# Performance work log

Measured on AMD Instinct MI355X. Metric: run time of the kernel, lower is better.

## Reference

```python
import jax, jax.numpy as jnp
import numpy as np

N_ATOMS = 50000
N_MOTIFS = 50000
N_INC = 600000
N_GRAPHS = 512
H = 64            # h_dim / node_fea_dim
MOTIF_DIM = 94    # motif hyperedge feature dim
HOUT = 128        # hout_dim
Z_DIM = 2 * H + MOTIF_DIM  # concat dim inside CHGConv
BN_EPS = 1e-5


def seg_mean(x, idx, num):
    s = jax.ops.segment_sum(x, idx, num_segments=num)
    c = jax.ops.segment_sum(jnp.ones((x.shape[0], 1), x.dtype), idx, num_segments=num)
    return s / jnp.maximum(c, 1.0)


def setup_inputs() -> dict:
    key = jax.random.key(0)
    ks = jax.random.split(key, 12)
    inp = {}
    inp['atom_z'] = jax.random.randint(ks[0], (N_ATOMS,), 0, 101)
    inp['motif_attr'] = jax.random.normal(ks[1], (N_MOTIFS, MOTIF_DIM), dtype=jnp.float32)
    inp['hyperedge_index'] = jax.random.randint(ks[2], (2, N_INC), 0, N_ATOMS)
    inp['batch'] = jnp.sort(jax.random.randint(ks[3], (N_ATOMS,), 0, N_GRAPHS))
    s = 0.05
    inp['embed_table'] = jax.random.normal(ks[4], (101, H), dtype=jnp.float32) * s
    inp['w_f'] = jax.random.normal(ks[5], (Z_DIM, H), dtype=jnp.float32) * s
    inp['b_f'] = jnp.zeros((H,), jnp.float32)
    inp['w_c'] = jax.random.normal(ks[6], (Z_DIM, H), dtype=jnp.float32) * s
    inp['b_c'] = jnp.zeros((H,), jnp.float32)
    inp['bn_gamma'] = jnp.ones((H,), jnp.float32)
    inp['bn_beta'] = jnp.zeros((H,), jnp.float32)
    inp['w_l1'] = jax.random.normal(ks[7], (H, HOUT), dtype=jnp.float32) * s
    inp['b_l1'] = jnp.zeros((HOUT,), jnp.float32)
    inp['w_out'] = jax.random.normal(ks[8], (HOUT, 1), dtype=jnp.float32) * s
    inp['b_out'] = jnp.zeros((1,), jnp.float32)
    return inp


def reference(atom_z, motif_attr, hyperedge_index, batch, embed_table,
              w_f, b_f, w_c, b_c, bn_gamma, bn_beta, w_l1, b_l1, w_out, b_out):
    # atom embedding lookup
    x = embed_table[atom_z]                       # [N_ATOMS, H]
    src = hyperedge_index[0]                      # atom indices per incidence
    hid = hyperedge_index[1]                      # motif hyperedge indices per incidence

    # CHGConv: aggregate node feats to hyperedges, gated CGCNN-style message, scatter back
    hx = seg_mean(x[src], hid, N_MOTIFS)          # [N_MOTIFS, H]
    z = jnp.concatenate([x[src], hx[hid], motif_attr[hid]], axis=1)  # [N_INC, 2H+94]
    msg = jax.nn.sigmoid(z @ w_f + b_f) * jax.nn.softplus(z @ w_c + b_c)
    out = seg_mean(msg, src, N_ATOMS)             # [N_ATOMS, H]

    # batch norm (training-mode batch stats) + residual, then outer relu
    mu = out.mean(0)
    var = out.var(0)
    out = (out - mu) / jnp.sqrt(var + BN_EPS) * bn_gamma + bn_beta
    x = jax.nn.relu(out + x)

    g = seg_mean(x, batch, N_GRAPHS)              # [N_GRAPHS, H]
    h = jax.nn.softplus(g @ w_l1 + b_l1)          # [N_GRAPHS, HOUT]
    return h @ w_out + b_out                      # [N_GRAPHS, 1]
```

## Files before the change

### kernel.cpp

```cpp
#include <hip/hip_runtime.h>
#include <hip/hip_bf16.h>
#include <hip/hip_fp16.h>
#include <math.h>

#define N_ATOMS  50000
#define N_MOTIFS 50000
#define N_SEG    (N_MOTIFS + N_ATOMS)
#define N_INC    600000
#define N_GRAPHS 512
#define H        64
#define MOTIF_DIM 94
#define KP       47
#define HOUT     128
#define BN_EPS   1e-5f
#define NZ       101
#define BCAP     64
#define NBINM    196
#define NBIN     392
#define BINCAP   4096
#define CHUNK    2048
#define NBLK_S   ((N_INC + CHUNK - 1) / CHUNK)
#define TL       16
#define NBLK_T   (N_MOTIFS / TL)
#define NREP     32

typedef _Float16 h2_t __attribute__((ext_vector_type(2)));
typedef float f32x2 __attribute__((ext_vector_type(2)));
__device__ __forceinline__ float fdot2(__half2 a, __half2 b, float c) {
    return __builtin_amdgcn_fdot2(*(h2_t*)&a, *(h2_t*)&b, c, false);
}

__device__ __forceinline__ float softplus_fast(float x) {
    return fmaxf(x, 0.0f) + __logf(1.0f + __expf(-fabsf(x)));
}
__device__ __forceinline__ float gate_f(float f, float c) {
    float sig = __builtin_amdgcn_rcpf(1.0f + __expf(-f));
    return sig * softplus_fast(c);
}

__global__ __launch_bounds__(256) void bin_scatter(const int* __restrict__ he,
                                                   const int* __restrict__ atom_z,
                                                   unsigned* __restrict__ bin_cnt,
                                                   unsigned* __restrict__ gbin) {
    __shared__ unsigned ecnt[NBIN];
    __shared__ unsigned ebase[NBIN];
    int tid = threadIdx.x;
    int e0 = blockIdx.x * CHUNK;
    int e1 = (e0 + CHUNK < N_INC) ? e0 + CHUNK : N_INC;
    for (int i = tid; i < NBIN; i += 256) ecnt[i] = 0;
    __syncthreads();
    for (int e = e0 + tid; e < e1; e += 256) {
        int s = he[e];
        int h = he[N_INC + e];
        atomicAdd(&ecnt[h >> 8], 1u);
        atomicAdd(&ecnt[NBINM + (s >> 8)], 1u);
    }
    __syncthreads();
    for (int i = tid; i < NBIN; i += 256) {
        unsigned c = ecnt[i];
        ebase[i] = c ? atomicAdd(&bin_cnt[i], c) : 0u;
        ecnt[i] = 0u;
    }
    __syncthreads();
    for (int e = e0 + tid; e < e1; e += 256) {
        int s = he[e];
        int h = he[N_INC + e];
        int az = atom_z[s];
        int bm = h >> 8;
        unsigned sm = ebase[bm] + atomicAdd(&ecnt[bm], 1u);
        if (sm < BINCAP)
            gbin[(size_t)bm * BINCAP + sm] = ((unsigned)(h & 255) << 16) | (unsigned)az;
        int ba = NBINM + (s >> 8);
        unsigned sa = ebase[ba] + atomicAdd(&ecnt[ba], 1u);
        if (sa < BINCAP)
            gbin[(size_t)ba * BINCAP + sa] = ((unsigned)(s & 255) << 16) | (unsigned)h;
    }
}

__global__ __launch_bounds__(256) void bin_build(const unsigned* __restrict__ bin_cnt,
                                                 const unsigned* __restrict__ gbin,
                                                 unsigned* __restrict__ cnt,
                                                 unsigned char* __restrict__ csr_m,
                                                 unsigned short* __restrict__ csr_a) {
    __shared__ unsigned short bkt[256 * BCAP];
    __shared__ unsigned cnts[256];
    int b = blockIdx.x;
    int tid = threadIdx.x;
    bool isM = b < NBINM;
    int seg0 = (isM ? b : (b - NBINM)) << 8;
    int lim = 50000 - seg0; if (lim > 256) lim = 256; if (lim < 0) lim = 0;
    cnts[tid] = 0u;
    __syncthreads();
    unsigned n = bin_cnt[b];
    if (n > BINCAP) n = BINCAP;
    for (unsigned k = tid; k < n; k += 256) {
        unsigned e = gbin[(size_t)b * BINCAP + k];
        unsigned loc = e >> 16, val = e & 0xFFFFu;
        unsigned slot = atomicAdd(&cnts[loc], 1u);
        if (slot < BCAP) bkt[loc * BCAP + slot] = (unsigned short)val;
    }
    __syncthreads();
    if (tid < lim) cnt[(isM ? seg0 : N_MOTIFS + seg0) + tid] = cnts[tid];
    if (isM) {
        for (int i = tid; i < lim * 16; i += 256) {
            int loc = i >> 4, w = i & 15;
            const unsigned short* sp = &bkt[loc * BCAP + 4 * w];
            unsigned v = (sp[0] & 0xffu) | ((sp[1] & 0xffu) << 8) |
                         ((sp[2] & 0xffu) << 16) | ((sp[3] & 0xffu) << 24);
            ((unsigned*)csr_m)[(size_t)(seg0 + loc) * 16 + w] = v;
        }
    } else {
        for (int i = tid; i < lim * 32; i += 256) {
            int loc = i >> 5, w = i & 31;
            const unsigned short* sp = &bkt[loc * BCAP + 2 * w];
            unsigned v = (unsigned)sp[0] | ((unsigned)sp[1] << 16);
            ((unsigned*)csr_a)[(size_t)(seg0 + loc) * 32 + w] = v;
        }
    }
}

__global__ __launch_bounds__(256) void aux_kernel(const float* __restrict__ table,
                                                  const float* __restrict__ w_f,
                                                  const float* __restrict__ w_c,
                                                  const float* __restrict__ b_f,
                                                  const float* __restrict__ b_c,
                                                  float* __restrict__ atab_fc,
                                                  __half* __restrict__ ptab_h,
                                                  __half2* __restrict__ w2_fc,
                                                  float* __restrict__ b_fc) {
    int t = threadIdx.x;
    int z = blockIdx.x;
    if (z >= NZ) {
        if (t < 128) {
            int sel = t & 1, col = t >> 1;
            b_fc[t] = (sel ? b_c : b_f)[col];
            const float* ws = sel ? w_c : w_f;
            for (int kp = 0; kp < KP; kp++)
                w2_fc[(size_t)kp * 128 + t] = __floats2half2_rn(
                    ws[(size_t)(2 * H + 2 * kp) * H + col],
                    ws[(size_t)(2 * H + 2 * kp + 1) * H + col]);
        }
        return;
    }
    __shared__ float trow[H];
    if (t < H) trow[t] = table[(size_t)z * H + t];
    __syncthreads();
    if (t < 128) {
        int sel = (t >= 64) ? 1 : 0;
        int jj = t & 63;
        const float* ws = sel ? w_c : w_f;
        float aacc = 0.0f, pacc = 0.0f;
        for (int k = 0; k < H; k++) {
            float tv = trow[k];
            aacc += tv * ws[(size_t)k * H + jj];
            pacc += tv * ws[(size_t)(H + k) * H + jj];
        }
        atab_fc[(size_t)z * 128 + jj * 2 + sel] = aacc;
        ptab_h[(size_t)z * 128 + jj * 2 + sel] = __float2half_rn(pacc);
    }
}

__global__ __launch_bounds__(256) void motif_fused(const unsigned* __restrict__ cnt,
                                                   const unsigned char* __restrict__ csr_m,
                                                   const __half2* __restrict__ ptab_h,
                                                   const float* __restrict__ motif_attr,
                                                   const __half2* __restrict__ w2_fc,
                                                   const float* __restrict__ b_fc,
                                                   __half2* __restrict__ m_fc) {
    __shared__ __half2 w_s[KP * 128];
    __shared__ __half2 z2[TL][KP];
    __shared__ int     ez[TL * BCAP];
    __shared__ float   invd[TL];
    __shared__ int     degs[TL];
    int tid = threadIdx.x;
    int m0 = blockIdx.x * TL;

    for (int k4 = tid; k4 < KP * 32; k4 += 256)
        ((uint4*)w_s)[k4] = ((const uint4*)w2_fc)[k4];
    {
        const int* src = (const int*)(csr_m + (size_t)m0 * BCAP);
        int w = src[tid];
        int b0 = tid * 4;
        ez[b0]     =  w        & 0xff;
        ez[b0 + 1] = (w >> 8)  & 0xff;
        ez[b0 + 2] = (w >> 16) & 0xff;
        ez[b0 + 3] = (w >> 24) & 0xff;
    }
    if (tid < TL) {
        int d = (int)cnt[m0 + tid];
        d = (d < BCAP) ? d : BCAP;
        degs[tid] = d;
        invd[tid] = 1.0f / fmaxf((float)d, 1.0f);
    }
    {
        const f32x2* ap = (const f32x2*)motif_attr;
        for (int idx = tid; idx < TL * KP; idx += 256) {
            int m = idx / KP, kp = idx % KP;
            f32x2 v = __builtin_nontemporal_load(&ap[(size_t)(m0 + m) * KP + kp]);
            z2[m][kp] = __floats2half2_rn(v.x, v.y);
        }
    }
    __syncthreads();

    const uint2* ptab_u2 = (const uint2*)ptab_h;
    int rg = tid >> 5;
    int cg = tid & 31;
    int q  = cg * 4;
    float4 bias4 = *(const float4*)(b_fc + q);

    float acc[2][4];
#pragma unroll
    for (int i = 0; i < 2; i++) {
        int r = rg * 2 + i;
        int lo = r * BCAP, d = degs[r];
        float g0 = 0.f, g1 = 0.f, g2 = 0.f, g3 = 0.f;
        int k = 0;
        for (; k + 8 <= d; k += 8) {
            int zz[8];
#pragma unroll
            for (int u = 0; u < 8; u++) zz[u] = ez[lo + k + u];
#pragma unroll
            for (int u = 0; u < 8; u++) {
                uint2 pr = ptab_u2[zz[u] * 32 + cg];
                float2 fa = __half22float2(*(__half2*)&pr.x);
                float2 fb = __half22float2(*(__half2*)&pr.y);
                g0 += fa.x; g1 += fa.y; g2 += fb.x; g3 += fb.y;
            }
        }
        for (; k < d; k++) {
            uint2 pr = ptab_u2[ez[lo + k] * 32 + cg];
            float2 fa = __half22float2(*(__half2*)&pr.x);
            float2 fb = __half22float2(*(__half2*)&pr.y);
            g0 += fa.x; g1 += fa.y; g2 += fb.x; g3 += fb.y;
        }
        float iv = invd[r];
        acc[i][0] = bias4.x + g0 * iv;
        acc[i][1] = bias4.y + g1 * iv;
        acc[i][2] = bias4.z + g2 * iv;
        acc[i][3] = bias4.w + g3 * iv;
    }

    {
        int r0 = rg * 2, r1 = r0 + 1;
#pragma unroll 4
        for (int kp = 0; kp < KP; kp++) {
            uint4 wr = *(const uint4*)(w_s + (size_t)kp * 128 + q);
            __half2 w0 = *(__half2*)&wr.x, w1 = *(__half2*)&wr.y;
            __half2 w2h = *(__half2*)&wr.z, w3 = *(__half2*)&wr.w;
            __half2 za = z2[r0][kp], zb = z2[r1][kp];
            acc[0][0] = fdot2(za, w0,  acc[0][0]);
            acc[0][1] = fdot2(za, w1,  acc[0][1]);
            acc[0][2] = fdot2(za, w2h, acc[0][2]);
            acc[0][3] = fdot2(za, w3,  acc[0][3]);
            acc[1][0] = fdot2(zb, w0,  acc[1][0]);
            acc[1][1] = fdot2(zb, w1,  acc[1][1]);
            acc[1][2] = fdot2(zb, w2h, acc[1][2]);
            acc[1][3] = fdot2(zb, w3,  acc[1][3]);
        }
    }
#pragma unroll
    for (int i = 0; i < 2; i++) {
        int gm = m0 + rg * 2 + i;
        m_fc[(size_t)gm * 64 + cg * 2]     = __floats2half2_rn(acc[i][0], acc[i][1]);
        m_fc[(size_t)gm * 64 + cg * 2 + 1] = __floats2half2_rn(acc[i][2], acc[i][3]);
    }
}

__global__ __launch_bounds__(256) void msg_gather(const unsigned* __restrict__ cnt,
                                                  const unsigned short* __restrict__ csr_a,
                                                  const int* __restrict__ atom_z,
                                                  const float2* __restrict__ atab_fc,
                                                  const __half2* __restrict__ m_fc,
                                                  float* __restrict__ out_mean,
                                                  float* __restrict__ bn_part) {
    int i = blockIdx.x * 4 + (threadIdx.x >> 6);
    int j = threadIdx.x & 63;
    int zi = __builtin_amdgcn_readfirstlane(atom_z[i]);
    float2 a = atab_fc[(size_t)zi * H + j];
    unsigned b = (unsigned)i * BCAP;
    int d = (int)__builtin_amdgcn_readfirstlane(cnt[N_MOTIFS + i]);
    d = (d < BCAP) ? d : BCAP;
    int dm1 = (d > 0) ? d - 1 : 0;
    float acc = 0.0f;
    for (int k = 0; k < d; k += 8) {
        int hh[8];
#pragma unroll
        for (int u = 0; u < 8; u++) {
            int o = k + u;
            hh[u] = (int)csr_a[b + (unsigned)((o < d) ? o : dm1)];
        }
        __half2 hv[8];
#pragma unroll
        for (int u = 0; u < 8; u++) hv[u] = m_fc[((unsigned)hh[u] << 6) + (unsigned)j];
#pragma unroll
        for (int u = 0; u < 8; u++)
            if (k + u < d) {
                float2 v = __half22float2(hv[u]);
                acc += gate_f(a.x + v.x, a.y + v.y);
            }
    }
    float v = acc / fmaxf((float)d, 1.0f);
    out_mean[(size_t)i * H + j] = v;
    __shared__ float ssum[256];
    __shared__ float ssq[256];
    ssum[threadIdx.x] = v; ssq[threadIdx.x] = v * v;
    __syncthreads();
    if (threadIdx.x < 64) {
        float* rep = bn_part + (size_t)(blockIdx.x & (NREP - 1)) * 128;
        atomicAdd(&rep[j],      ssum[j] + ssum[64 + j] + ssum[128 + j] + ssum[192 + j]);
        atomicAdd(&rep[64 + j], ssq[j]  + ssq[64 + j]  + ssq[128 + j]  + ssq[192 + j]);
    }
}

__global__ __launch_bounds__(256) void pool_head(const float* __restrict__ out_mean,
                                                 const float* __restrict__ bn_part,
                                                 const float* __restrict__ gamma,
                                                 const float* __restrict__ beta,
                                                 const int* __restrict__ atom_z,
                                                 const float* __restrict__ table,
                                                 const int* __restrict__ batch,
                                                 const float* __restrict__ w_l1,
                                                 const float* __restrict__ b_l1,
                                                 const float* __restrict__ w_out,
                                                 const float* __restrict__ b_out,
                                                 float* __restrict__ out) {
    int g = blockIdx.x;
    int tid = threadIdx.x;
    __shared__ int bounds[2];
    __shared__ float red[256];
    __shared__ float gv[H];
    __shared__ float red2[HOUT];
    __shared__ float bnred[128];
    if (tid < 2) {
        int target = g + tid;
        int lo = 0, hi = N_ATOMS;
        while (lo < hi) {
            int mid = (lo + hi) >> 1;
            if (batch[mid] < target) lo = mid + 1; else hi = mid;
        }
        bounds[tid] = lo;
    }
    if (tid < 128) {
        float s = 0.0f;
        for (int r = 0; r < NREP; r++) s += bn_part[(size_t)r * 128 + tid];
        bnred[tid] = s;
    }
    __syncthreads();
    int s = bounds[0], e = bounds[1];
    int j = tid & 63, w = tid >> 6;
    const float invN = 1.0f / (float)N_ATOMS;
    float mu = bnred[j] * invN;
    float var = bnred[64 + j] * invN - mu * mu;
    float rstd = 1.0f / sqrtf(var + BN_EPS);
    float gm = gamma[j], bt = beta[j];
    float acc = 0.0f;
    for (int i = s + w; i < e; i += 4) {
        float d = out_mean[(size_t)i * H + j];
        float xv = table[(size_t)atom_z[i] * H + j];
        float o = (d - mu) * rstd * gm + bt;
        acc += fmaxf(o + xv, 0.0f);
    }
    red[tid] = acc;
    __syncthreads();
    if (tid < 64)
        gv[j] = (red[j] + red[64 + j] + red[128 + j] + red[192 + j])
                / fmaxf((float)(e - s), 1.0f);
    __syncthreads();
    if (tid < HOUT) {
        float a2 = b_l1[tid];
        for (int k = 0; k < H; k++) a2 += gv[k] * w_l1[(size_t)k * HOUT + tid];
        red2[tid] = softplus_fast(a2) * w_out[tid];
    }
    __syncthreads();
    for (int st = 64; st > 0; st >>= 1) {
        if (tid < st) red2[tid] += red2[tid + st];
        __syncthreads();
    }
    if (tid == 0) out[g] = red2[0] + b_out[0];
}

extern "C" void kernel_launch(void* const* d_in, const int* in_sizes, int n_in,
                              void* d_out, int out_size, void* d_ws, size_t ws_size,
                              hipStream_t stream) {
    const int*   atom_z     = (const int*)  d_in[0];
    const float* motif_attr = (const float*)d_in[1];
    const int*   he         = (const int*)  d_in[2];
    const int*   batch      = (const int*)  d_in[3];
    const float* table      = (const float*)d_in[4];
    const float* w_f        = (const float*)d_in[5];
    const float* b_f        = (const float*)d_in[6];
    const float* w_c        = (const float*)d_in[7];
    const float* b_c        = (const float*)d_in[8];
    const float* gamma      = (const float*)d_in[9];
    const float* beta       = (const float*)d_in[10];
    const float* w_l1       = (const float*)d_in[11];
    const float* b_l1       = (const float*)d_in[12];
    const float* w_out      = (const float*)d_in[13];
    const float* b_out      = (const float*)d_in[14];
    float* out = (float*)d_out;

    float*    bn_part = (float*)d_ws;
    unsigned* bin_cnt = (unsigned*)(bn_part + NREP * 128);
    char*     zero_end = (char*)(bin_cnt + 400);
    unsigned* cnt     = (unsigned*)zero_end;
    unsigned* gbin    = cnt + N_SEG;
    unsigned char*  csr_m = (unsigned char*)(gbin + (size_t)NBIN * BINCAP);
    unsigned short* csr_a = (unsigned short*)(csr_m + (size_t)N_MOTIFS * BCAP);
    float*    atab_fc  = (float*)(csr_a + (size_t)N_ATOMS * BCAP);
    __half*   ptab_h   = (__half*)(atab_fc + (size_t)NZ * 128);
    __half2*  w2_fc    = (__half2*)(ptab_h + (size_t)NZ * 128);
    float*    b_fc     = (float*)(w2_fc + (size_t)KP * 128);
    __half2*  m_fc     = (__half2*)(b_fc + 128);
    float*    out_mean = (float*)(m_fc + (size_t)N_MOTIFS * 64);

    size_t zero_bytes = (size_t)(zero_end - (char*)d_ws);
    hipMemsetAsync(d_ws, 0, zero_bytes, stream);

    aux_kernel<<<NZ + 1, 256, 0, stream>>>(table, w_f, w_c, b_f, b_c,
                                           atab_fc, ptab_h, w2_fc, b_fc);
    bin_scatter<<<NBLK_S, 256, 0, stream>>>(he, atom_z, bin_cnt, gbin);
    bin_build<<<NBIN, 256, 0, stream>>>(bin_cnt, gbin, cnt, csr_m, csr_a);
    motif_fused<<<NBLK_T, 256, 0, stream>>>(cnt, csr_m, (const __half2*)ptab_h,
                                            motif_attr, w2_fc, b_fc, m_fc);
    msg_gather<<<N_ATOMS / 4, 256, 0, stream>>>(cnt, csr_a, atom_z,
                                                (const float2*)atab_fc,
                                                m_fc, out_mean, bn_part);
    pool_head<<<N_GRAPHS, 256, 0, stream>>>(out_mean, bn_part, gamma, beta,
                                            atom_z, table, batch,
                                            w_l1, b_l1, w_out, b_out, out);
}
```

Baseline: 228.1 us.

## Fuse aux precompute into bin scatter and use base-2 gate math

The separate aux_kernel launch is folded into the bin_scatter kernel as extra blocks, removing one kernel launch and its serialization. The gate/weight tables are pre-scaled by log2(e) so the message gate can use native exp2/log2 intrinsics, with a final multiply by ln2 applied once per atom. The gather loop also predicates the index and message loads instead of clamping to the last valid index. The pre-scaling changes fp16 rounding slightly. Motif_fused must consume the scaled tables consistently, and that code is not shown.

```diff
diff --git a/kernel.cpp b/kernel.cpp
--- a/kernel.cpp
+++ b/kernel.cpp
@@ -23,6 +23,8 @@
 #define TL       16
 #define NBLK_T   (N_MOTIFS / TL)
 #define NREP     32
+#define LOG2E    1.44269504088896f
+#define LN2      0.69314718055995f
 
 typedef _Float16 h2_t __attribute__((ext_vector_type(2)));
 typedef float f32x2 __attribute__((ext_vector_type(2)));
@@ -33,18 +35,62 @@
 __device__ __forceinline__ float softplus_fast(float x) {
     return fmaxf(x, 0.0f) + __logf(1.0f + __expf(-fabsf(x)));
 }
-__device__ __forceinline__ float gate_f(float f, float c) {
-    float sig = __builtin_amdgcn_rcpf(1.0f + __expf(-f));
-    return sig * softplus_fast(c);
-}
-
-__global__ __launch_bounds__(256) void bin_scatter(const int* __restrict__ he,
-                                                   const int* __restrict__ atom_z,
-                                                   unsigned* __restrict__ bin_cnt,
-                                                   unsigned* __restrict__ gbin) {
+__device__ __forceinline__ float gate2(float f, float c) {
+    float e   = __builtin_amdgcn_exp2f(-f);
+    float sig = __builtin_amdgcn_rcpf(1.0f + e);
+    float ec  = __builtin_amdgcn_exp2f(-fabsf(c));
+    float sp  = fmaxf(c, 0.0f) + __builtin_amdgcn_logf(1.0f + ec);
+    return sig * sp;
+}
+
+__global__ __launch_bounds__(256) void bin_scatter_aux(const int* __restrict__ he,
+                                                       const int* __restrict__ atom_z,
+                                                       unsigned* __restrict__ bin_cnt,
+                                                       unsigned* __restrict__ gbin,
+                                                       const float* __restrict__ table,
+                                                       const float* __restrict__ w_f,
+                                                       const float* __restrict__ w_c,
+                                                       const float* __restrict__ b_f,
+                                                       const float* __restrict__ b_c,
+                                                       float* __restrict__ atab_fc,
+                                                       __half* __restrict__ ptab_h,
+                                                       __half2* __restrict__ w2_fc,
+                                                       float* __restrict__ b_fc) {
     __shared__ unsigned ecnt[NBIN];
     __shared__ unsigned ebase[NBIN];
+    __shared__ float trow[H];
     int tid = threadIdx.x;
+    if (blockIdx.x >= NBLK_S) {
+        int z = blockIdx.x - NBLK_S;
+        if (z >= NZ) {
+            if (tid < 128) {
+                int sel = tid & 1, col = tid >> 1;
+                b_fc[tid] = (sel ? b_c : b_f)[col] * LOG2E;
+                const float* ws = sel ? w_c : w_f;
+                for (int kp = 0; kp < KP; kp++)
+                    w2_fc[(size_t)kp * 128 + tid] = __floats2half2_rn(
+                        ws[(size_t)(2 * H + 2 * kp) * H + col] * LOG2E,
+                        ws[(size_t)(2 * H + 2 * kp + 1) * H + col] * LOG2E);
+            }
+            return;
+        }
+        if (tid < H) trow[tid] = table[(size_t)z * H + tid];
+        __syncthreads();
+        if (tid < 128) {
+            int sel = (tid >= 64) ? 1 : 0;
+            int jj = tid & 63;
+            const float* ws = sel ? w_c : w_f;
+            float aacc = 0.0f, pacc = 0.0f;
+            for (int k = 0; k < H; k++) {
+                float tv = trow[k];
+                aacc += tv * ws[(size_t)k * H + jj];
+                pacc += tv * ws[(size_t)(H + k) * H + jj];
+            }
+            atab_fc[(size_t)z * 128 + jj * 2 + sel] = aacc * LOG2E;
+            ptab_h[(size_t)z * 128 + jj * 2 + sel] = __float2half_rn(pacc * LOG2E);
+        }
+        return;
+    }
     int e0 = blockIdx.x * CHUNK;
     int e1 = (e0 + CHUNK < N_INC) ? e0 + CHUNK : N_INC;
     for (int i = tid; i < NBIN; i += 256) ecnt[i] = 0;
@@ -116,47 +162,6 @@
             unsigned v = (unsigned)sp[0] | ((unsigned)sp[1] << 16);
             ((unsigned*)csr_a)[(size_t)(seg0 + loc) * 32 + w] = v;
         }
-    }
-}
-
-__global__ __launch_bounds__(256) void aux_kernel(const float* __restrict__ table,
-                                                  const float* __restrict__ w_f,
-                                                  const float* __restrict__ w_c,
-                                                  const float* __restrict__ b_f,
-                                                  const float* __restrict__ b_c,
-                                                  float* __restrict__ atab_fc,
-                                                  __half* __restrict__ ptab_h,
-                                                  __half2* __restrict__ w2_fc,
-                                                  float* __restrict__ b_fc) {
-    int t = threadIdx.x;
-    int z = blockIdx.x;
-    if (z >= NZ) {
-        if (t < 128) {
-            int sel = t & 1, col = t >> 1;
-            b_fc[t] = (sel ? b_c : b_f)[col];
-            const float* ws = sel ? w_c : w_f;
-            for (int kp = 0; kp < KP; kp++)
-                w2_fc[(size_t)kp * 128 + t] = __floats2half2_rn(
-                    ws[(size_t)(2 * H + 2 * kp) * H + col],
-                    ws[(size_t)(2 * H + 2 * kp + 1) * H + col]);
-        }
-        return;
-    }
-    __shared__ float trow[H];
-    if (t < H) trow[t] = table[(size_t)z * H + t];
-    __syncthreads();
-    if (t < 128) {
-        int sel = (t >= 64) ? 1 : 0;
-        int jj = t & 63;
-        const float* ws = sel ? w_c : w_f;
-        float aacc = 0.0f, pacc = 0.0f;
-        for (int k = 0; k < H; k++) {
-            float tv = trow[k];
-            aacc += tv * ws[(size_t)k * H + jj];
-            pacc += tv * ws[(size_t)(H + k) * H + jj];
-        }
-        atab_fc[(size_t)z * 128 + jj * 2 + sel] = aacc;
-        ptab_h[(size_t)z * 128 + jj * 2 + sel] = __float2half_rn(pacc);
     }
 }
 
@@ -280,26 +285,24 @@
     unsigned b = (unsigned)i * BCAP;
     int d = (int)__builtin_amdgcn_readfirstlane(cnt[N_MOTIFS + i]);
     d = (d < BCAP) ? d : BCAP;
-    int dm1 = (d > 0) ? d - 1 : 0;
     float acc = 0.0f;
     for (int k = 0; k < d; k += 8) {
         int hh[8];
-#pragma unroll
-        for (int u = 0; u < 8; u++) {
-            int o = k + u;
-            hh[u] = (int)csr_a[b + (unsigned)((o < d) ? o : dm1)];
-        }
         __half2 hv[8];
 #pragma unroll
-        for (int u = 0; u < 8; u++) hv[u] = m_fc[((unsigned)hh[u] << 6) + (unsigned)j];
+        for (int u = 0; u < 8; u++)
+            if (k + u < d) hh[u] = (int)csr_a[b + (unsigned)(k + u)];
+#pragma unroll
+        for (int u = 0; u < 8; u++)
+            if (k + u < d) hv[u] = m_fc[((unsigned)hh[u] << 6) + (unsigned)j];
 #pragma unroll
         for (int u = 0; u < 8; u++)
             if (k + u < d) {
                 float2 v = __half22float2(hv[u]);
-                acc += gate_f(a.x + v.x, a.y + v.y);
+                acc += gate2(a.x + v.x, a.y + v.y);
             }
     }
-    float v = acc / fmaxf((float)d, 1.0f);
+    float v = (acc * LN2) / fmaxf((float)d, 1.0f);
     out_mean[(size_t)i * H + j] = v;
     __shared__ float ssum[256];
     __shared__ float ssq[256];
@@ -416,9 +419,9 @@
     size_t zero_bytes = (size_t)(zero_end - (char*)d_ws);
     hipMemsetAsync(d_ws, 0, zero_bytes, stream);
 
-    aux_kernel<<<NZ + 1, 256, 0, stream>>>(table, w_f, w_c, b_f, b_c,
-                                           atab_fc, ptab_h, w2_fc, b_fc);
-    bin_scatter<<<NBLK_S, 256, 0, stream>>>(he, atom_z, bin_cnt, gbin);
+    bin_scatter_aux<<<NBLK_S + NZ + 1, 256, 0, stream>>>(he, atom_z, bin_cnt, gbin,
+                                                         table, w_f, w_c, b_f, b_c,
+                                                         atab_fc, ptab_h, w2_fc, b_fc);
     bin_build<<<NBIN, 256, 0, stream>>>(bin_cnt, gbin, cnt, csr_m, csr_a);
     motif_fused<<<NBLK_T, 256, 0, stream>>>(cnt, csr_m, (const __half2*)ptab_h,
                                             motif_attr, w2_fc, b_fc, m_fc);
```

Result: no change. 231.4 us (+1.4%).
